# Kernel optimization log

Measured on AMD Instinct MI355X. Metric: run time of the kernel, lower is better.

## Reference

```python
import jax, jax.numpy as jnp
import numpy as np

EPS = 1e-5

def _ln(x, g, b):
    mu = jnp.mean(x, axis=-1, keepdims=True)
    var = jnp.mean((x - mu) ** 2, axis=-1, keepdims=True)
    return (x - mu) * jax.lax.rsqrt(var + EPS) * g + b

def _block(x, W1, b1, g1, be1, W2, b2, g2, be2):
    # Linear -> LN -> ReLU -> Linear -> LN -> ReLU
    h = jax.nn.relu(_ln(x @ W1 + b1, g1, be1))
    return jax.nn.relu(_ln(h @ W2 + b2, g2, be2))

def setup_inputs() -> dict:
    key = jax.random.key(0)
    ks = jax.random.split(key, 10)
    B, N, P, C, H, O = 32, 512, 20, 13, 128, 256
    inp = {
        'polylines': jax.random.normal(ks[0], (B, N, P, C), dtype=jnp.float32),
        'polylines_mask': jax.random.randint(ks[1], (B, N, P), 0, 2) > 0,
        # fc1
        'fc1_W1': jax.random.normal(ks[2], (C, H), jnp.float32) * (1.0 / np.sqrt(C)),
        'fc1_b1': jnp.zeros((H,), jnp.float32),
        'fc1_g1': jnp.ones((H,), jnp.float32), 'fc1_be1': jnp.zeros((H,), jnp.float32),
        'fc1_W2': jax.random.normal(ks[3], (H, H), jnp.float32) * (1.0 / np.sqrt(H)),
        'fc1_b2': jnp.zeros((H,), jnp.float32),
        'fc1_g2': jnp.ones((H,), jnp.float32), 'fc1_be2': jnp.zeros((H,), jnp.float32),
        # fc2 (input is 2*H after concat with pooled feature)
        'fc2_W1': jax.random.normal(ks[4], (2 * H, H), jnp.float32) * (1.0 / np.sqrt(2 * H)),
        'fc2_b1': jnp.zeros((H,), jnp.float32),
        'fc2_g1': jnp.ones((H,), jnp.float32), 'fc2_be1': jnp.zeros((H,), jnp.float32),
        'fc2_W2': jax.random.normal(ks[5], (H, H), jnp.float32) * (1.0 / np.sqrt(H)),
        'fc2_b2': jnp.zeros((H,), jnp.float32),
        'fc2_g2': jnp.ones((H,), jnp.float32), 'fc2_be2': jnp.zeros((H,), jnp.float32),
        # fc_out: Linear -> ReLU -> Linear
        'fo_W1': jax.random.normal(ks[6], (H, H), jnp.float32) * (1.0 / np.sqrt(H)),
        'fo_b1': jnp.zeros((H,), jnp.float32),
        'fo_W2': jax.random.normal(ks[7], (H, O), jnp.float32) * (1.0 / np.sqrt(H)),
        'fo_b2': jnp.zeros((O,), jnp.float32),
    }
    return inp

def reference(polylines, polylines_mask,
              fc1_W1, fc1_b1, fc1_g1, fc1_be1, fc1_W2, fc1_b2, fc1_g2, fc1_be2,
              fc2_W1, fc2_b1, fc2_g1, fc2_be1, fc2_W2, fc2_b2, fc2_g2, fc2_be2,
              fo_W1, fo_b1, fo_W2, fo_b2):
    # Equivalent to torch's mask-gather/scatter-into-zeros: compute everywhere,
    # zero out invalid points. Invalid slots are exactly 0, so max over points matches.
    m = polylines_mask[..., None].astype(polylines.dtype)  # [B,N,P,1]
    feat = _block(polylines, fc1_W1, fc1_b1, fc1_g1, fc1_be1,
                  fc1_W2, fc1_b2, fc1_g2, fc1_be2) * m       # [B,N,P,H]
    pooled = jnp.max(feat, axis=2)                            # [B,N,H]
    P = feat.shape[2]
    cat = jnp.concatenate(
        [feat, jnp.broadcast_to(pooled[:, :, None, :], feat.shape)], axis=-1)  # [B,N,P,2H]
    feat2 = _block(cat, fc2_W1, fc2_b1, fc2_g1, fc2_be1,
                   fc2_W2, fc2_b2, fc2_g2, fc2_be2) * m       # [B,N,P,H]
    pooled2 = jnp.max(feat2, axis=2)                          # [B,N,H]
    valid = jnp.any(polylines_mask, axis=-1)                  # [B,N]
    out = (jax.nn.relu(pooled2 @ fo_W1 + fo_b1) @ fo_W2 + fo_b2)
    return out * valid[..., None].astype(out.dtype)           # [B,N,O]
```

## Files before the change

kernel.cpp:

```cpp
#include <hip/hip_runtime.h>
#include <math.h>


#define PP 20
#define HH 128
#define OO 256
#define NW 16
#define PSTR 136

typedef __fp16   fp16x2 __attribute__((ext_vector_type(2)));
typedef _Float16 f16x4 __attribute__((ext_vector_type(4)));
typedef _Float16 f16x8 __attribute__((ext_vector_type(8)));
typedef float    f32x4 __attribute__((ext_vector_type(4)));

__device__ __forceinline__ f32x4 splat4(float x) { f32x4 v = {x, x, x, x}; return v; }

__device__ __forceinline__ f32x4 max4(f32x4 a, f32x4 b)
{
#if __has_builtin(__builtin_elementwise_max)
  return __builtin_elementwise_max(a, b);
#else
  f32x4 r;
  r[0] = fmaxf(a[0], b[0]); r[1] = fmaxf(a[1], b[1]);
  r[2] = fmaxf(a[2], b[2]); r[3] = fmaxf(a[3], b[3]);
  return r;
#endif
}

__device__ __forceinline__ f32x4 MFMA(f16x8 a, f16x8 b, f32x4 c)
{
  return __builtin_amdgcn_mfma_f32_16x16x32_f16(a, b, c, 0, 0, 0);
}

__device__ __forceinline__ f16x8 ldfrag2(const _Float16* p)
{
  f16x8 r;
  f16x4* r4 = reinterpret_cast<f16x4*>(&r);
  r4[0] = *reinterpret_cast<const f16x4*>(p);
  r4[1] = *reinterpret_cast<const f16x4*>(p + 16);
  return r;
}

__device__ __forceinline__ f16x8 pack8(const f32x4 a, const f32x4 b)
{
  union { fp16x2 h2[4]; f16x8 h8; } u;
  u.h2[0] = __builtin_amdgcn_cvt_pkrtz(a[0], a[1]);
  u.h2[1] = __builtin_amdgcn_cvt_pkrtz(a[2], a[3]);
  u.h2[2] = __builtin_amdgcn_cvt_pkrtz(b[0], b[1]);
  u.h2[3] = __builtin_amdgcn_cvt_pkrtz(b[2], b[3]);
  return u.h8;
}

template<int KSROW>
__device__ __forceinline__ void gemm_ks(const _Float16* wbase, int ks,
                                        const f16x8 bf0, const f16x8 bf1,
                                        f32x4 acc[8][2], int lane)
{
#pragma unroll
  for (int nt = 0; nt < 8; nt++) {
    const f16x8 wf = *(const f16x8*)(wbase + (size_t)(nt * KSROW + ks) * 512 + lane * 8);
    acc[nt][0] = MFMA(wf, bf0, acc[nt][0]);
    acc[nt][1] = MFMA(wf, bf1, acc[nt][1]);
  }
}

__device__ __forceinline__ void zero_acc(f32x4 acc[8][2])
{
#pragma unroll
  for (int nt = 0; nt < 8; nt++) { acc[nt][0] = splat4(0.f); acc[nt][1] = splat4(0.f); }
}

template<bool DOMASKPOOL>
__device__ __forceinline__ void ln_blk(f32x4 acc[8][2],
                                       const float* __restrict__ bv,
                                       const float* __restrict__ gv,
                                       const float* __restrict__ bev,
                                       float mf0, float mf1,
                                       f32x4 pm[8], int lg)
{
  f32x4 sv0 = splat4(0.f), sv1 = splat4(0.f), qv0 = splat4(0.f), qv1 = splat4(0.f);
#pragma unroll
  for (int nt = 0; nt < 8; nt++) {
    const f32x4 bb = *(const f32x4*)(bv + 16 * nt + 4 * lg);
    f32x4 v0 = acc[nt][0] + bb;
    f32x4 v1 = acc[nt][1] + bb;
    acc[nt][0] = v0;  acc[nt][1] = v1;
    sv0 += v0;  qv0 = v0 * v0 + qv0;
    sv1 += v1;  qv1 = v1 * v1 + qv1;
  }
  float mu[2], rs[2];
#pragma unroll
  for (int mt = 0; mt < 2; mt++) {
    const f32x4 sv = mt ? sv1 : sv0;
    const f32x4 qv = mt ? qv1 : qv0;
    float s = (sv[0] + sv[1]) + (sv[2] + sv[3]);
    float q = (qv[0] + qv[1]) + (qv[2] + qv[3]);
    s += __shfl_xor(s, 16, 64); s += __shfl_xor(s, 32, 64);
    q += __shfl_xor(q, 16, 64); q += __shfl_xor(q, 32, 64);
    mu[mt] = s * (1.f / 128.f);
    rs[mt] = rsqrtf(fmaxf(q * (1.f / 128.f) - mu[mt] * mu[mt], 0.f) + 1e-5f);
  }
  const f32x4 z4 = splat4(0.f);
  const f32x4 rs0 = splat4(rs[0]),           rs1 = splat4(rs[1]);
  const f32x4 nm0 = splat4(-mu[0] * rs[0]),  nm1 = splat4(-mu[1] * rs[1]);
  const f32x4 m0  = splat4(mf0),             m1  = splat4(mf1);
#pragma unroll
  for (int nt = 0; nt < 8; nt++) {
    const f32x4 g4  = *(const f32x4*)(gv  + 16 * nt + 4 * lg);
    const f32x4 be4 = *(const f32x4*)(bev + 16 * nt + 4 * lg);
    f32x4 t0 = acc[nt][0] * rs0 + nm0;
    f32x4 t1 = acc[nt][1] * rs1 + nm1;
    f32x4 v0 = max4(t0 * g4 + be4, z4);
    f32x4 v1 = max4(t1 * g4 + be4, z4);
    if (DOMASKPOOL) {
      v0 = v0 * m0;
      v1 = v1 * m1;
      pm[nt] = max4(pm[nt], max4(v0, v1));
    }
    acc[nt][0] = v0;  acc[nt][1] = v1;
  }
}

__global__ void prep_weights(const float* __restrict__ W1, const float* __restrict__ W2,
                             const float* __restrict__ F2W1, const float* __restrict__ F2W2,
                             const float* __restrict__ FO1, const float* __restrict__ FO2,
                             _Float16* __restrict__ wt)
{
  const int idx = blockIdx.x * 256 + threadIdx.x;
  if (idx >= 118784) return;
  float v;
  if (idx < 69632) {
    const int jj = idx & 7;
    const int lane = (idx >> 3) & 63;
    const int fg = idx >> 9;
    const int l15 = lane & 15, lg = lane >> 4;
    const int kin = 4 * lg + (jj & 3) + ((jj & 4) << 2);
    if (fg < 8)        { const int n = fg * 16 + l15;                  v = (kin < 13) ? W1[kin * 128 + n] : 0.f; }
    else if (fg < 40)  { const int f = fg - 8;   const int n = (f >> 2) * 16 + l15, k = (f & 3) * 32 + kin; v = W2[k * 128 + n]; }
    else if (fg < 104) { const int f = fg - 40;  const int n = (f >> 3) * 16 + l15, k = (f & 7) * 32 + kin; v = F2W1[k * 128 + n]; }
    else               { const int f = fg - 104; const int n = (f >> 2) * 16 + l15, k = (f & 3) * 32 + kin; v = F2W2[k * 128 + n]; }
  } else if (idx < 86016) { const int j = idx - 69632; const int n = j >> 7, k = j & 127; v = FO1[k * 128 + n]; }
  else                    { const int j = idx - 86016; const int n = j >> 7, k = j & 127; v = FO2[k * 256 + n]; }
  wt[idx] = (_Float16)v;
}

extern "C" __global__ void __launch_bounds__(1024, 1)
polynet_main(const float* __restrict__ poly, const int* __restrict__ maskp,
             const float* __restrict__ b1,  const float* __restrict__ g1,  const float* __restrict__ be1,
             const float* __restrict__ b2,  const float* __restrict__ g2,  const float* __restrict__ be2,
             const float* __restrict__ f2b1, const float* __restrict__ f2g1, const float* __restrict__ f2be1,
             const float* __restrict__ f2b2, const float* __restrict__ f2g2, const float* __restrict__ f2be2,
             const _Float16* __restrict__ wt,
             _Float16* __restrict__ pooled2h, float* __restrict__ vldw)
{
  __shared__ _Float16 ldsw[69632];
  __shared__ _Float16 ldsp[NW][HH];

  const int tid  = threadIdx.x;
  const int lane = tid & 63;
  const int w    = tid >> 6;
  const int l15  = lane & 15;
  const int lg   = lane >> 4;
  const int pid  = blockIdx.x * NW + w;

  {
    const uint4* src = (const uint4*)wt;
    uint4* dst = (uint4*)ldsw;
    for (int i = tid; i < 8704; i += 1024) dst[i] = src[i];
  }

  int mrow = 0;
  if (lane < PP) mrow = maskp[(size_t)pid * PP + lane];
  const float vld = (__ballot(mrow != 0) != 0ULL) ? 1.f : 0.f;
  const int mi0 = __shfl(mrow, l15, 64);
  const int mi1 = __shfl(mrow, 16 + l15, 64);
  const float mf0 = (mi0 != 0) ? 1.f : 0.f;
  const float mf1 = (l15 < 4 && mi1 != 0) ? 1.f : 0.f;

  const float* xp = poly + (size_t)pid * (PP * 13);
  f16x8 x0, x1;
#pragma unroll
  for (int jj = 0; jj < 4; jj++) {
    const int k = 4 * lg + jj;
    const float v0 = (k < 13) ? xp[l15 * 13 + k] : 0.f;
    const float v1 = (k < 13 && l15 < 4) ? xp[(16 + l15) * 13 + k] : 0.f;
    x0[jj] = (_Float16)v0;  x0[4 + jj] = (_Float16)0.f;
    x1[jj] = (_Float16)v1;  x1[4 + jj] = (_Float16)0.f;
  }

  __syncthreads();

  const _Float16* wtL1 = ldsw;
  const _Float16* wtL2 = ldsw + 4096;
  const _Float16* wtL3 = ldsw + 20480;
  const _Float16* wtL4 = ldsw + 53248;

  f32x4 acc[8][2];
  f16x8 Hf0[4], Hf1[4];
  f32x4 pm[8];

  zero_acc(acc);
  gemm_ks<1>(wtL1, 0, x0, x1, acc, lane);
  ln_blk<false>(acc, b1, g1, be1, mf0, mf1, pm, lg);
#pragma unroll
  for (int ks = 0; ks < 4; ks++) {
    Hf0[ks] = pack8(acc[2 * ks][0], acc[2 * ks + 1][0]);
    Hf1[ks] = pack8(acc[2 * ks][1], acc[2 * ks + 1][1]);
  }

  zero_acc(acc);
#pragma unroll
  for (int ks = 0; ks < 4; ks++) gemm_ks<4>(wtL2, ks, Hf0[ks], Hf1[ks], acc, lane);
#pragma unroll
  for (int nt = 0; nt < 8; nt++) pm[nt] = splat4(0.f);
  ln_blk<true>(acc, b2, g2, be2, mf0, mf1, pm, lg);
#pragma unroll
  for (int nt = 0; nt < 8; nt++)
#pragma unroll
    for (int j = 0; j < 4; j++) {
      float p = pm[nt][j];
      p = fmaxf(p, __shfl_xor(p, 1, 64));
      p = fmaxf(p, __shfl_xor(p, 2, 64));
      p = fmaxf(p, __shfl_xor(p, 4, 64));
      p = fmaxf(p, __shfl_xor(p, 8, 64));
      pm[nt][j] = p;
    }
  f16x8 Pf[4];
#pragma unroll
  for (int ks = 0; ks < 4; ks++) Pf[ks] = pack8(pm[2 * ks], pm[2 * ks + 1]);
#pragma unroll
  for (int ks = 0; ks < 4; ks++) {
    Hf0[ks] = pack8(acc[2 * ks][0], acc[2 * ks + 1][0]);
    Hf1[ks] = pack8(acc[2 * ks][1], acc[2 * ks + 1][1]);
  }

  zero_acc(acc);
#pragma unroll
  for (int ks = 0; ks < 4; ks++) gemm_ks<8>(wtL3, ks, Hf0[ks], Hf1[ks], acc, lane);
#pragma unroll
  for (int ks = 4; ks < 8; ks++) gemm_ks<8>(wtL3, ks, Pf[ks - 4], Pf[ks - 4], acc, lane);
  ln_blk<false>(acc, f2b1, f2g1, f2be1, mf0, mf1, pm, lg);
#pragma unroll
  for (int ks = 0; ks < 4; ks++) {
    Hf0[ks] = pack8(acc[2 * ks][0], acc[2 * ks + 1][0]);
    Hf1[ks] = pack8(acc[2 * ks][1], acc[2 * ks + 1][1]);
  }

  zero_acc(acc);
#pragma unroll
  for (int ks = 0; ks < 4; ks++) gemm_ks<4>(wtL4, ks, Hf0[ks], Hf1[ks], acc, lane);
#pragma unroll
  for (int nt = 0; nt < 8; nt++) pm[nt] = splat4(0.f);
  ln_blk<true>(acc, f2b2, f2g2, f2be2, mf0, mf1, pm, lg);
#pragma unroll
  for (int nt = 0; nt < 8; nt++)
#pragma unroll
    for (int j = 0; j < 4; j++) {
      float p = pm[nt][j];
      p = fmaxf(p, __shfl_xor(p, 1, 64));
      p = fmaxf(p, __shfl_xor(p, 2, 64));
      p = fmaxf(p, __shfl_xor(p, 4, 64));
      p = fmaxf(p, __shfl_xor(p, 8, 64));
      pm[nt][j] = p;
    }

  if (l15 == 0) {
#pragma unroll
    for (int nt = 0; nt < 8; nt++)
#pragma unroll
      for (int j = 0; j < 4; j++)
        ldsp[w][nt * 16 + 4 * lg + j] = (_Float16)pm[nt][j];
  }
  const unsigned int pv = *(const unsigned int*)(&ldsp[w][lane * 2]);
  *(unsigned int*)(pooled2h + (size_t)pid * HH + lane * 2) = pv;
  if (lane == 0) vldw[pid] = vld;
}

extern "C" __global__ void __launch_bounds__(256, 2)
k_head(const _Float16* __restrict__ pooled2h, const float* __restrict__ vldw,
       const _Float16* __restrict__ wt,
       const float* __restrict__ fob1, const float* __restrict__ fob2,
       float* __restrict__ out)
{
  __shared__ _Float16 Z1[64 * PSTR];
  const int tid = threadIdx.x, lane = tid & 63, w = tid >> 6;
  const int l15 = lane & 15, lg = lane >> 4;
  const int rbase = blockIdx.x * 64;

  const _Float16* FOW1t = wt + 69632;
  const _Float16* FOW2t = wt + 86016;

  {
    f32x4 az[4][2];
    const float bz0 = fob1[32 * w + l15];
    const float bz1 = fob1[32 * w + 16 + l15];
#pragma unroll
    for (int mt = 0; mt < 4; mt++) { az[mt][0] = splat4(bz0); az[mt][1] = splat4(bz1); }
    f16x8 bfr[2][4];
#pragma unroll
    for (int nt = 0; nt < 2; nt++) {
      const _Float16* bp = FOW1t + (size_t)((2 * w + nt) * 16 + l15) * 128 + 4 * lg;
#pragma unroll
      for (int ks = 0; ks < 4; ks++) bfr[nt][ks] = ldfrag2(bp + 32 * ks);
    }
#pragma unroll
    for (int mt = 0; mt < 4; mt++) {
      const _Float16* ap = pooled2h + (size_t)(rbase + mt * 16 + l15) * HH + 4 * lg;
#pragma unroll
      for (int ks = 0; ks < 4; ks++) {
        f16x8 a = ldfrag2(ap + 32 * ks);
        az[mt][0] = MFMA(a, bfr[0][ks], az[mt][0]);
        az[mt][1] = MFMA(a, bfr[1][ks], az[mt][1]);
      }
    }
#pragma unroll
    for (int mt = 0; mt < 4; mt++)
#pragma unroll
      for (int j = 0; j < 4; j++) {
        const int row = mt * 16 + lg * 4 + j;
        Z1[row * PSTR + 32 * w + l15]      = (_Float16)fmaxf(az[mt][0][j], 0.f);
        Z1[row * PSTR + 32 * w + 16 + l15] = (_Float16)fmaxf(az[mt][1][j], 0.f);
      }
  }
  __syncthreads();

  {
    f16x8 a[4][4];
#pragma unroll
    for (int mt = 0; mt < 4; mt++)
#pragma unroll
      for (int ks = 0; ks < 4; ks++)
        a[mt][ks] = ldfrag2(Z1 + (mt * 16 + l15) * PSTR + 4 * lg + 32 * ks);
    f32x4 o[4][4];
#pragma unroll
    for (int nt = 0; nt < 4; nt++) {
      const int c = (4 * w + nt) * 16 + l15;
      const float bo = fob2[c];
#pragma unroll
      for (int mt = 0; mt < 4; mt++) o[mt][nt] = splat4(bo);
      const _Float16* bp = FOW2t + (size_t)((4 * w + nt) * 16 + l15) * 128 + 4 * lg;
#pragma unroll
      for (int ks = 0; ks < 4; ks++) {
        f16x8 b = ldfrag2(bp + 32 * ks);
#pragma unroll
        for (int mt = 0; mt < 4; mt++) o[mt][nt] = MFMA(a[mt][ks], b, o[mt][nt]);
      }
    }
#pragma unroll
    for (int mt = 0; mt < 4; mt++)
#pragma unroll
      for (int j = 0; j < 4; j++) {
        const int row = mt * 16 + lg * 4 + j;
        const float v = vldw[rbase + row];
#pragma unroll
        for (int nt = 0; nt < 4; nt++)
          out[(size_t)(rbase + row) * OO + (4 * w + nt) * 16 + l15] = o[mt][nt][j] * v;
      }
  }
}

extern "C" void kernel_launch(void* const* d_in, const int* in_sizes, int n_in,
                              void* d_out, int out_size, void* d_ws, size_t ws_size,
                              hipStream_t stream)
{
  const float* poly  = (const float*)d_in[0];
  const int*   mask  = (const int*)d_in[1];
  const float* W1    = (const float*)d_in[2];
  const float* b1    = (const float*)d_in[3];
  const float* g1    = (const float*)d_in[4];
  const float* be1   = (const float*)d_in[5];
  const float* W2    = (const float*)d_in[6];
  const float* b2    = (const float*)d_in[7];
  const float* g2    = (const float*)d_in[8];
  const float* be2   = (const float*)d_in[9];
  const float* f2W1  = (const float*)d_in[10];
  const float* f2b1  = (const float*)d_in[11];
  const float* f2g1  = (const float*)d_in[12];
  const float* f2be1 = (const float*)d_in[13];
  const float* f2W2  = (const float*)d_in[14];
  const float* f2b2  = (const float*)d_in[15];
  const float* f2g2  = (const float*)d_in[16];
  const float* f2be2 = (const float*)d_in[17];
  const float* foW1  = (const float*)d_in[18];
  const float* fob1  = (const float*)d_in[19];
  const float* foW2  = (const float*)d_in[20];
  const float* fob2  = (const float*)d_in[21];
  float* out = (float*)d_out;

  const int npoly = in_sizes[0] / (PP * 13);

  char* ws = (char*)d_ws;
  _Float16* wt       = (_Float16*)ws;
  _Float16* pooled2h = (_Float16*)(ws + 237568);
  float*    vldw     = (float*)(ws + 237568 + (size_t)npoly * HH * 2);

  prep_weights<<<dim3((118784 + 255) / 256), dim3(256), 0, stream>>>(
      W1, W2, f2W1, f2W2, foW1, foW2, wt);

  polynet_main<<<dim3(npoly / NW), dim3(1024), 0, stream>>>(
      poly, mask, b1, g1, be1, b2, g2, be2,
      f2b1, f2g1, f2be1, f2b2, f2g2, f2be2,
      wt, pooled2h, vldw);

  k_head<<<dim3(npoly / 64), dim3(256), 0, stream>>>(
      pooled2h, vldw, wt, fob1, fob2, out);
}
```

Before: 155.2 us.

## Pack two polylines per wave into three MFMA row tiles to cut padding

Each wavefront now processes two polylines (40 points) using three 16-row MFMA tiles instead of one polyline padded to 32 rows. The mixed third tile holds 4 points from each polyline, and masked pooling is split with per-lane selectors. This reduces wasted padded MFMA work and reuses each loaded weight fragment across three MFMAs instead of two. The block shrinks to 512 threads, and register pressure rises, which may hurt occupancy given the large LDS footprint.

```diff
diff --git a/kernel.cpp b/kernel.cpp
--- a/kernel.cpp
+++ b/kernel.cpp
@@ -5,7 +5,6 @@
 #define PP 20
 #define HH 128
 #define OO 256
-#define NW 16
 #define PSTR 136
 
 typedef __fp16   fp16x2 __attribute__((ext_vector_type(2)));
@@ -51,73 +50,92 @@
   return u.h8;
 }
 
+__device__ __forceinline__ f16x8 sel8(bool c, const f16x8 a, const f16x8 b)
+{
+  union { f16x8 h; uint4 u; } ua, ub, ur;
+  ua.h = a; ub.h = b;
+  ur.u.x = c ? ua.u.x : ub.u.x;
+  ur.u.y = c ? ua.u.y : ub.u.y;
+  ur.u.z = c ? ua.u.z : ub.u.z;
+  ur.u.w = c ? ua.u.w : ub.u.w;
+  return ur.h;
+}
+
 template<int KSROW>
-__device__ __forceinline__ void gemm_ks(const _Float16* wbase, int ks,
-                                        const f16x8 bf0, const f16x8 bf1,
-                                        f32x4 acc[8][2], int lane)
+__device__ __forceinline__ void gemm3(const _Float16* wbase, int ks,
+                                      const f16x8 b0, const f16x8 b1, const f16x8 b2,
+                                      f32x4 acc[8][3], int lane)
 {
 #pragma unroll
   for (int nt = 0; nt < 8; nt++) {
     const f16x8 wf = *(const f16x8*)(wbase + (size_t)(nt * KSROW + ks) * 512 + lane * 8);
-    acc[nt][0] = MFMA(wf, bf0, acc[nt][0]);
-    acc[nt][1] = MFMA(wf, bf1, acc[nt][1]);
-  }
-}
-
-__device__ __forceinline__ void zero_acc(f32x4 acc[8][2])
-{
-#pragma unroll
-  for (int nt = 0; nt < 8; nt++) { acc[nt][0] = splat4(0.f); acc[nt][1] = splat4(0.f); }
+    acc[nt][0] = MFMA(wf, b0, acc[nt][0]);
+    acc[nt][1] = MFMA(wf, b1, acc[nt][1]);
+    acc[nt][2] = MFMA(wf, b2, acc[nt][2]);
+  }
+}
+
+__device__ __forceinline__ void zero_acc3(f32x4 acc[8][3])
+{
+#pragma unroll
+  for (int nt = 0; nt < 8; nt++) {
+    acc[nt][0] = splat4(0.f); acc[nt][1] = splat4(0.f); acc[nt][2] = splat4(0.f);
+  }
 }
 
 template<bool DOMASKPOOL>
-__device__ __forceinline__ void ln_blk(f32x4 acc[8][2],
-                                       const float* __restrict__ bv,
-                                       const float* __restrict__ gv,
-                                       const float* __restrict__ bev,
-                                       float mf0, float mf1,
-                                       f32x4 pm[8], int lg)
-{
-  f32x4 sv0 = splat4(0.f), sv1 = splat4(0.f), qv0 = splat4(0.f), qv1 = splat4(0.f);
+__device__ __forceinline__ void ln3(f32x4 acc[8][3],
+                                    const float* __restrict__ bv,
+                                    const float* __restrict__ gv,
+                                    const float* __restrict__ bev,
+                                    const f32x4 mfv[3],
+                                    f32x4 pmA[8], f32x4 pmB[8],
+                                    const f32x4 selA, const f32x4 selB, int lg)
+{
+  f32x4 sv[3], qv[3];
+#pragma unroll
+  for (int t = 0; t < 3; t++) { sv[t] = splat4(0.f); qv[t] = splat4(0.f); }
 #pragma unroll
   for (int nt = 0; nt < 8; nt++) {
     const f32x4 bb = *(const f32x4*)(bv + 16 * nt + 4 * lg);
-    f32x4 v0 = acc[nt][0] + bb;
-    f32x4 v1 = acc[nt][1] + bb;
-    acc[nt][0] = v0;  acc[nt][1] = v1;
-    sv0 += v0;  qv0 = v0 * v0 + qv0;
-    sv1 += v1;  qv1 = v1 * v1 + qv1;
-  }
-  float mu[2], rs[2];
-#pragma unroll
-  for (int mt = 0; mt < 2; mt++) {
-    const f32x4 sv = mt ? sv1 : sv0;
-    const f32x4 qv = mt ? qv1 : qv0;
-    float s = (sv[0] + sv[1]) + (sv[2] + sv[3]);
-    float q = (qv[0] + qv[1]) + (qv[2] + qv[3]);
+#pragma unroll
+    for (int t = 0; t < 3; t++) {
+      f32x4 v = acc[nt][t] + bb;
+      acc[nt][t] = v;
+      sv[t] += v;
+      qv[t] = v * v + qv[t];
+    }
+  }
+  float mu[3], rs[3];
+#pragma unroll
+  for (int t = 0; t < 3; t++) {
+    float s = (sv[t][0] + sv[t][1]) + (sv[t][2] + sv[t][3]);
+    float q = (qv[t][0] + qv[t][1]) + (qv[t][2] + qv[t][3]);
     s += __shfl_xor(s, 16, 64); s += __shfl_xor(s, 32, 64);
     q += __shfl_xor(q, 16, 64); q += __shfl_xor(q, 32, 64);
-    mu[mt] = s * (1.f / 128.f);
-    rs[mt] = rsqrtf(fmaxf(q * (1.f / 128.f) - mu[mt] * mu[mt], 0.f) + 1e-5f);
+    mu[t] = s * (1.f / 128.f);
+    rs[t] = rsqrtf(fmaxf(q * (1.f / 128.f) - mu[t] * mu[t], 0.f) + 1e-5f);
   }
   const f32x4 z4 = splat4(0.f);
-  const f32x4 rs0 = splat4(rs[0]),           rs1 = splat4(rs[1]);
-  const f32x4 nm0 = splat4(-mu[0] * rs[0]),  nm1 = splat4(-mu[1] * rs[1]);
-  const f32x4 m0  = splat4(mf0),             m1  = splat4(mf1);
+  f32x4 rsv[3], nmv[3];
+#pragma unroll
+  for (int t = 0; t < 3; t++) { rsv[t] = splat4(rs[t]); nmv[t] = splat4(-mu[t] * rs[t]); }
 #pragma unroll
   for (int nt = 0; nt < 8; nt++) {
     const f32x4 g4  = *(const f32x4*)(gv  + 16 * nt + 4 * lg);
     const f32x4 be4 = *(const f32x4*)(bev + 16 * nt + 4 * lg);
-    f32x4 t0 = acc[nt][0] * rs0 + nm0;
-    f32x4 t1 = acc[nt][1] * rs1 + nm1;
-    f32x4 v0 = max4(t0 * g4 + be4, z4);
-    f32x4 v1 = max4(t1 * g4 + be4, z4);
-    if (DOMASKPOOL) {
-      v0 = v0 * m0;
-      v1 = v1 * m1;
-      pm[nt] = max4(pm[nt], max4(v0, v1));
-    }
-    acc[nt][0] = v0;  acc[nt][1] = v1;
+#pragma unroll
+    for (int t = 0; t < 3; t++) {
+      f32x4 tt = acc[nt][t] * rsv[t] + nmv[t];
+      f32x4 v = max4(tt * g4 + be4, z4);
+      if (DOMASKPOOL) {
+        v = v * mfv[t];
+        if (t == 0)      pmA[nt] = max4(pmA[nt], v);
+        else if (t == 1) pmB[nt] = max4(pmB[nt], v);
+        else { pmA[nt] = max4(pmA[nt], v * selA); pmB[nt] = max4(pmB[nt], v * selB); }
+      }
+      acc[nt][t] = v;
+    }
   }
 }
 
@@ -144,7 +162,7 @@
   wt[idx] = (_Float16)v;
 }
 
-extern "C" __global__ void __launch_bounds__(1024, 1)
+extern "C" __global__ void __launch_bounds__(512, 2)
 polynet_main(const float* __restrict__ poly, const int* __restrict__ maskp,
              const float* __restrict__ b1,  const float* __restrict__ g1,  const float* __restrict__ be1,
              const float* __restrict__ b2,  const float* __restrict__ g2,  const float* __restrict__ be2,
@@ -154,38 +172,53 @@
              _Float16* __restrict__ pooled2h, float* __restrict__ vldw)
 {
   __shared__ _Float16 ldsw[69632];
-  __shared__ _Float16 ldsp[NW][HH];
+  __shared__ _Float16 ldsp[16][HH];
 
   const int tid  = threadIdx.x;
   const int lane = tid & 63;
   const int w    = tid >> 6;
   const int l15  = lane & 15;
   const int lg   = lane >> 4;
-  const int pid  = blockIdx.x * NW + w;
+  const int pidA = blockIdx.x * 16 + 2 * w;
+  const int pidB = pidA + 1;
 
   {
     const uint4* src = (const uint4*)wt;
     uint4* dst = (uint4*)ldsw;
-    for (int i = tid; i < 8704; i += 1024) dst[i] = src[i];
+    for (int i = tid; i < 8704; i += 512) dst[i] = src[i];
   }
 
   int mrow = 0;
-  if (lane < PP) mrow = maskp[(size_t)pid * PP + lane];
-  const float vld = (__ballot(mrow != 0) != 0ULL) ? 1.f : 0.f;
+  if (lane < PP)                 mrow = maskp[(size_t)pidA * PP + lane];
+  else if (lane >= 32 && lane < 32 + PP) mrow = maskp[(size_t)pidB * PP + (lane - 32)];
+  const float vldA = (__ballot(lane < PP && mrow != 0) != 0ULL) ? 1.f : 0.f;
+  const float vldB = (__ballot(lane >= 32 && mrow != 0) != 0ULL) ? 1.f : 0.f;
   const int mi0 = __shfl(mrow, l15, 64);
-  const int mi1 = __shfl(mrow, 16 + l15, 64);
-  const float mf0 = (mi0 != 0) ? 1.f : 0.f;
-  const float mf1 = (l15 < 4 && mi1 != 0) ? 1.f : 0.f;
-
-  const float* xp = poly + (size_t)pid * (PP * 13);
-  f16x8 x0, x1;
+  const int mi1 = __shfl(mrow, 32 + l15, 64);
+  const int mi2 = __shfl(mrow, (l15 < 4) ? (16 + l15) : (44 + l15), 64);
+  f32x4 mfv[3];
+  mfv[0] = splat4((mi0 != 0) ? 1.f : 0.f);
+  mfv[1] = splat4((mi1 != 0) ? 1.f : 0.f);
+  mfv[2] = splat4((l15 < 8 && mi2 != 0) ? 1.f : 0.f);
+  const f32x4 selA = splat4((l15 < 4) ? 1.f : 0.f);
+  const f32x4 selB = splat4((l15 >= 4 && l15 < 8) ? 1.f : 0.f);
+
+  const float* xp = poly + (size_t)pidA * (PP * 13);
+  const float* xq = poly + (size_t)pidB * (PP * 13);
+  f16x8 x0, x1, x2;
 #pragma unroll
   for (int jj = 0; jj < 4; jj++) {
     const int k = 4 * lg + jj;
-    const float v0 = (k < 13) ? xp[l15 * 13 + k] : 0.f;
-    const float v1 = (k < 13 && l15 < 4) ? xp[(16 + l15) * 13 + k] : 0.f;
+    float v0 = 0.f, v1 = 0.f, v2 = 0.f;
+    if (k < 13) {
+      v0 = xp[l15 * 13 + k];
+      v1 = xq[l15 * 13 + k];
+      if (l15 < 4)      v2 = xp[(16 + l15) * 13 + k];
+      else if (l15 < 8) v2 = xq[(12 + l15) * 13 + k];
+    }
     x0[jj] = (_Float16)v0;  x0[4 + jj] = (_Float16)0.f;
     x1[jj] = (_Float16)v1;  x1[4 + jj] = (_Float16)0.f;
+    x2[jj] = (_Float16)v2;  x2[4 + jj] = (_Float16)0.f;
   }
 
   __syncthreads();
@@ -195,85 +228,108 @@
   const _Float16* wtL3 = ldsw + 20480;
   const _Float16* wtL4 = ldsw + 53248;
 
-  f32x4 acc[8][2];
-  f16x8 Hf0[4], Hf1[4];
-  f32x4 pm[8];
-
-  zero_acc(acc);
-  gemm_ks<1>(wtL1, 0, x0, x1, acc, lane);
-  ln_blk<false>(acc, b1, g1, be1, mf0, mf1, pm, lg);
+  f32x4 acc[8][3];
+  f16x8 Hf0[4], Hf1[4], Hf2[4];
+  f32x4 pmA[8], pmB[8];
+
+  zero_acc3(acc);
+  gemm3<1>(wtL1, 0, x0, x1, x2, acc, lane);
+  ln3<false>(acc, b1, g1, be1, mfv, pmA, pmB, selA, selB, lg);
 #pragma unroll
   for (int ks = 0; ks < 4; ks++) {
     Hf0[ks] = pack8(acc[2 * ks][0], acc[2 * ks + 1][0]);
     Hf1[ks] = pack8(acc[2 * ks][1], acc[2 * ks + 1][1]);
-  }
-
-  zero_acc(acc);
-#pragma unroll
-  for (int ks = 0; ks < 4; ks++) gemm_ks<4>(wtL2, ks, Hf0[ks], Hf1[ks], acc, lane);
-#pragma unroll
-  for (int nt = 0; nt < 8; nt++) pm[nt] = splat4(0.f);
-  ln_blk<true>(acc, b2, g2, be2, mf0, mf1, pm, lg);
+    Hf2[ks] = pack8(acc[2 * ks][2], acc[2 * ks + 1][2]);
+  }
+
+  zero_acc3(acc);
+#pragma unroll
+  for (int ks = 0; ks < 4; ks++) gemm3<4>(wtL2, ks, Hf0[ks], Hf1[ks], Hf2[ks], acc, lane);
+#pragma unroll
+  for (int nt = 0; nt < 8; nt++) { pmA[nt] = splat4(0.f); pmB[nt] = splat4(0.f); }
+  ln3<true>(acc, b2, g2, be2, mfv, pmA, pmB, selA, selB, lg);
 #pragma unroll
   for (int nt = 0; nt < 8; nt++)
 #pragma unroll
     for (int j = 0; j < 4; j++) {
-      float p = pm[nt][j];
+      float p = pmA[nt][j];
       p = fmaxf(p, __shfl_xor(p, 1, 64));
       p = fmaxf(p, __shfl_xor(p, 2, 64));
       p = fmaxf(p, __shfl_xor(p, 4, 64));
       p = fmaxf(p, __shfl_xor(p, 8, 64));
-      pm[nt][j] = p;
-    }
-  f16x8 Pf[4];
-#pragma unroll
-  for (int ks = 0; ks < 4; ks++) Pf[ks] = pack8(pm[2 * ks], pm[2 * ks + 1]);
+      pmA[nt][j] = p;
+      float q = pmB[nt][j];
+      q = fmaxf(q, __shfl_xor(q, 1, 64));
+      q = fmaxf(q, __shfl_xor(q, 2, 64));
+      q = fmaxf(q, __shfl_xor(q, 4, 64));
+      q = fmaxf(q, __shfl_xor(q, 8, 64));
+      pmB[nt][j] = q;
+    }
+  f16x8 PfA[4], PfB[4], Pf2[4];
+#pragma unroll
+  for (int ks = 0; ks < 4; ks++) {
+    PfA[ks] = pack8(pmA[2 * ks], pmA[2 * ks + 1]);
+    PfB[ks] = pack8(pmB[2 * ks], pmB[2 * ks + 1]);
+    Pf2[ks] = sel8(l15 < 4, PfA[ks], PfB[ks]);
+  }
 #pragma unroll
   for (int ks = 0; ks < 4; ks++) {
     Hf0[ks] = pack8(acc[2 * ks][0], acc[2 * ks + 1][0]);
     Hf1[ks] = pack8(acc[2 * ks][1], acc[2 * ks + 1][1]);
-  }
-
-  zero_acc(acc);
-#pragma unroll
-  for (int ks = 0; ks < 4; ks++) gemm_ks<8>(wtL3, ks, Hf0[ks], Hf1[ks], acc, lane);
-#pragma unroll
-  for (int ks = 4; ks < 8; ks++) gemm_ks<8>(wtL3, ks, Pf[ks - 4], Pf[ks - 4], acc, lane);
-  ln_blk<false>(acc, f2b1, f2g1, f2be1, mf0, mf1, pm, lg);
+    Hf2[ks] = pack8(acc[2 * ks][2], acc[2 * ks + 1][2]);
+  }
+
+  zero_acc3(acc);
+#pragma unroll
+  for (int ks = 0; ks < 4; ks++) gemm3<8>(wtL3, ks, Hf0[ks], Hf1[ks], Hf2[ks], acc, lane);
+#pragma unroll
+  for (int ks = 4; ks < 8; ks++) gemm3<8>(wtL3, ks, PfA[ks - 4], PfB[ks - 4], Pf2[ks - 4], acc, lane);
+  ln3<false>(acc, f2b1, f2g1, f2be1, mfv, pmA, pmB, selA, selB, lg);
 #pragma unroll
   for (int ks = 0; ks < 4; ks++) {
     Hf0[ks] = pack8(acc[2 * ks][0], acc[2 * ks + 1][0]);
     Hf1[ks] = pack8(acc[2 * ks][1], acc[2 * ks + 1][1]);
-  }
-
-  zero_acc(acc);
-#pragma unroll
-  for (int ks = 0; ks < 4; ks++) gemm_ks<4>(wtL4, ks, Hf0[ks], Hf1[ks], acc, lane);
-#pragma unroll
-  for (int nt = 0; nt < 8; nt++) pm[nt] = splat4(0.f);
-  ln_blk<true>(acc, f2b2, f2g2, f2be2, mf0, mf1, pm, lg);
+    Hf2[ks] = pack8(acc[2 * ks][2], acc[2 * ks + 1][2]);
+  }
+
+  zero_acc3(acc);
+#pragma unroll
+  for (int ks = 0; ks < 4; ks++) gemm3<4>(wtL4, ks, Hf0[ks], Hf1[ks], Hf2[ks], acc, lane);
+#pragma unroll
+  for (int nt = 0; nt < 8; nt++) { pmA[nt] = splat4(0.f); pmB[nt] = splat4(0.f); }
+  ln3<true>(acc, f2b2, f2g2, f2be2, mfv, pmA, pmB, selA, selB, lg);
 #pragma unroll
   for (int nt = 0; nt < 8; nt++)
 #pragma unroll
     for (int j = 0; j < 4; j++) {
-      float p = pm[nt][j];
+      float p = pmA[nt][j];
       p = fmaxf(p, __shfl_xor(p, 1, 64));
       p = fmaxf(p, __shfl_xor(p, 2, 64));
       p = fmaxf(p, __shfl_xor(p, 4, 64));
       p = fmaxf(p, __shfl_xor(p, 8, 64));
-      pm[nt][j] = p;
+      pmA[nt][j] = p;
+      float q = pmB[nt][j];
+      q = fmaxf(q, __shfl_xor(q, 1, 64));
+      q = fmaxf(q, __shfl_xor(q, 2, 64));
+      q = fmaxf(q, __shfl_xor(q, 4, 64));
+      q = fmaxf(q, __shfl_xor(q, 8, 64));
+      pmB[nt][j] = q;
     }
 
   if (l15 == 0) {
 #pragma unroll
     for (int nt = 0; nt < 8; nt++)
 #pragma unroll
-      for (int j = 0; j < 4; j++)
-        ldsp[w][nt * 16 + 4 * lg + j] = (_Float16)pm[nt][j];
-  }
-  const unsigned int pv = *(const unsigned int*)(&ldsp[w][lane * 2]);
-  *(unsigned int*)(pooled2h + (size_t)pid * HH + lane * 2) = pv;
-  if (lane == 0) vldw[pid] = vld;
+      for (int j = 0; j < 4; j++) {
+        ldsp[2 * w][nt * 16 + 4 * lg + j]     = (_Float16)pmA[nt][j];
+        ldsp[2 * w + 1][nt * 16 + 4 * lg + j] = (_Float16)pmB[nt][j];
+      }
+  }
+  const unsigned int pvA = *(const unsigned int*)(&ldsp[2 * w][lane * 2]);
+  const unsigned int pvB = *(const unsigned int*)(&ldsp[2 * w + 1][lane * 2]);
+  *(unsigned int*)(pooled2h + (size_t)pidA * HH + lane * 2) = pvA;
+  *(unsigned int*)(pooled2h + (size_t)pidB * HH + lane * 2) = pvB;
+  if (lane == 0) { vldw[pidA] = vldA; vldw[pidB] = vldB; }
 }
 
 extern "C" __global__ void __launch_bounds__(256, 2)
@@ -397,7 +453,7 @@
   prep_weights<<<dim3((118784 + 255) / 256), dim3(256), 0, stream>>>(
       W1, W2, f2W1, f2W2, foW1, foW2, wt);
 
-  polynet_main<<<dim3(npoly / NW), dim3(1024), 0, stream>>>(
+  polynet_main<<<dim3(npoly / 16), dim3(512), 0, stream>>>(
       poly, mask, b1, g1, be1, b2, g2, be2,
       f2b1, f2g1, f2be1, f2b2, f2g2, f2be2,
       wt, pooled2h, vldw);
```

Measured after the change: 158.8 us. 2.3% more time.
